# Kernel optimization log

Measured on AMD Instinct MI355X. Metric: run time of the kernel, lower is better.

Reference implementation:

```python
import jax, jax.numpy as jnp
import numpy as np

B, S, D_IN, D_OUT, H = 4, 2048, 1024, 1024, 16
HD = D_OUT // H


def setup_inputs() -> dict:
    key = jax.random.key(0)
    ks = jax.random.split(key, 6)
    s_in = 1.0 / np.sqrt(D_IN)
    s_out = 1.0 / np.sqrt(D_OUT)
    return {
        "x": jax.random.normal(ks[0], (B, S, D_IN), dtype=jnp.float32),
        "Wq": jax.random.uniform(ks[1], (D_IN, D_OUT), jnp.float32, -s_in, s_in),
        "Wk": jax.random.uniform(ks[2], (D_IN, D_OUT), jnp.float32, -s_in, s_in),
        "Wv": jax.random.uniform(ks[3], (D_IN, D_OUT), jnp.float32, -s_in, s_in),
        "Wo": jax.random.uniform(ks[4], (D_OUT, D_OUT), jnp.float32, -s_out, s_out),
        "bo": jax.random.uniform(ks[5], (D_OUT,), jnp.float32, -s_out, s_out),
    }


def reference(x, Wq, Wk, Wv, Wo, bo):
    b, s, _ = x.shape
    # project and split heads: (b, h, s, hd)
    def heads(w):
        return (x @ w).reshape(b, s, H, HD).transpose(0, 2, 1, 3)
    q, k, v = heads(Wq), heads(Wk), heads(Wv)
    scores = jnp.einsum("bhqd,bhkd->bhqk", q, k) / np.sqrt(HD).astype(np.float32)
    causal = jnp.tril(jnp.ones((s, s), dtype=bool))  # True = keep
    scores = jnp.where(causal, scores, -jnp.inf)
    attn = jax.nn.softmax(scores, axis=-1)
    ctx = jnp.einsum("bhqk,bhkd->bhqd", attn, v)
    ctx = ctx.transpose(0, 2, 1, 3).reshape(b, s, D_OUT)
    return ctx @ Wo.T + bo
```

## Files before the change

kernel.cpp:

```cpp
#include <hip/hip_runtime.h>
#include <hip/hip_bf16.h>

#define BB   4
#define SS   2048
#define DIN  1024
#define DOUT 1024
#define NH   16
#define HDIM 64

typedef __hip_bfloat16 bf16;
typedef __attribute__((ext_vector_type(8))) short short8;
typedef __attribute__((ext_vector_type(4))) float floatx4;

#define AS1(p) ((const __attribute__((address_space(1))) void*)(p))
#define AS3(p) ((__attribute__((address_space(3))) void*)(p))

__global__ void cast_f32_bf16_kernel(const float* __restrict__ src, bf16* __restrict__ dst) {
    size_t i = ((size_t)blockIdx.x * 256 + threadIdx.x) * 8;
    float4 a = *(const float4*)(src + i);
    float4 b = *(const float4*)(src + i + 4);
    bf16 o[8] __attribute__((aligned(16)));
    o[0] = __float2bfloat16(a.x); o[1] = __float2bfloat16(a.y);
    o[2] = __float2bfloat16(a.z); o[3] = __float2bfloat16(a.w);
    o[4] = __float2bfloat16(b.x); o[5] = __float2bfloat16(b.y);
    o[6] = __float2bfloat16(b.z); o[7] = __float2bfloat16(b.w);
    *(short8*)(dst + i) = *(short8*)o;
}

__global__ void prep_wqkv_kernel(const float* __restrict__ Wq, const float* __restrict__ Wk,
                                 const float* __restrict__ Wv, bf16* __restrict__ wt) {
    __shared__ float tile[64][65];
    const int kt = blockIdx.x;
    const int nt = blockIdx.y;
    const int k0 = kt * 64, n0 = nt * 64;
    const float* W = (n0 < 1024) ? Wq : (n0 < 2048 ? Wk : Wv);
    const int col0 = n0 & 1023;
    const int tid = threadIdx.x;
    {
        const int kl = tid >> 2, nc = (tid & 3) * 16;
        const float* src = W + (size_t)(k0 + kl) * 1024 + col0 + nc;
        #pragma unroll
        for (int i = 0; i < 16; i += 4) {
            float4 v = *(const float4*)(src + i);
            tile[kl][nc + i + 0] = v.x; tile[kl][nc + i + 1] = v.y;
            tile[kl][nc + i + 2] = v.z; tile[kl][nc + i + 3] = v.w;
        }
    }
    __syncthreads();
    {
        const int nl = tid >> 2, kc = (tid & 3) * 16;
        bf16 o[16] __attribute__((aligned(16)));
        #pragma unroll
        for (int i = 0; i < 16; ++i) o[i] = __float2bfloat16(tile[kc + i][nl]);
        bf16* dst = wt + (size_t)(n0 + nl) * 1024 + k0 + kc;
        *(short8*)dst       = *(short8*)&o[0];
        *(short8*)(dst + 8) = *(short8*)&o[8];
    }
}

template<int EPI>
__global__ __launch_bounds__(256) void gemm_bt_kernel(
    const bf16* __restrict__ A, const bf16* __restrict__ Bt,
    void* __restrict__ C, const float* __restrict__ bias, int K, int ldc) {
    __shared__ __align__(16) bf16 As[128][32];
    __shared__ __align__(16) bf16 Bs[128][32];
    const int tid  = threadIdx.x;
    const int wave = tid >> 6, lane = tid & 63;
    const int lm   = lane & 15, quad = lane >> 4;
    const int wm   = (wave >> 1) * 64, wn = (wave & 1) * 64;
    const size_t rowA0 = (size_t)blockIdx.x * 128;
    const size_t rowB0 = (size_t)blockIdx.y * 128;
    const int srow = wave * 16 + (lane >> 2);
    const int skc  = (lane & 3) * 8;

    floatx4 acc[4][4] = {};

    for (int k0 = 0; k0 < K; k0 += 32) {
        __syncthreads();
        #pragma unroll
        for (int r = 0; r < 2; ++r) {
            const bf16* gA = A  + (rowA0 + r * 64 + srow) * (size_t)K + k0 + skc;
            __builtin_amdgcn_global_load_lds(AS1(gA), AS3(&As[r * 64 + wave * 16][0]), 16, 0, 0);
            const bf16* gB = Bt + (rowB0 + r * 64 + srow) * (size_t)K + k0 + skc;
            __builtin_amdgcn_global_load_lds(AS1(gB), AS3(&Bs[r * 64 + wave * 16][0]), 16, 0, 0);
        }
        __syncthreads();
        short8 a[4], b[4];
        #pragma unroll
        for (int i = 0; i < 4; ++i) a[i] = *(const short8*)&As[wm + i * 16 + lm][quad * 8];
        #pragma unroll
        for (int j = 0; j < 4; ++j) b[j] = *(const short8*)&Bs[wn + j * 16 + lm][quad * 8];
        #pragma unroll
        for (int i = 0; i < 4; ++i)
            #pragma unroll
            for (int j = 0; j < 4; ++j)
                acc[i][j] = __builtin_amdgcn_mfma_f32_16x16x32_bf16(a[i], b[j], acc[i][j], 0, 0, 0);
    }

    #pragma unroll
    for (int i = 0; i < 4; ++i) {
        size_t row = rowA0 + wm + i * 16 + quad * 4;
        #pragma unroll
        for (int j = 0; j < 4; ++j) {
            size_t col = rowB0 + wn + j * 16 + lm;
            float bv = (EPI == 1) ? bias[col] : 0.0f;
            #pragma unroll
            for (int r = 0; r < 4; ++r) {
                if (EPI == 0)
                    ((bf16*)C)[(row + r) * ldc + col] = __float2bfloat16(acc[i][j][r]);
                else
                    ((float*)C)[(row + r) * ldc + col] = acc[i][j][r] + bv;
            }
        }
    }
}

__global__ void transpose_v_kernel(const bf16* __restrict__ qkv, bf16* __restrict__ vt) {
    __shared__ __align__(16) bf16 tile[64][72];
    const int st = blockIdx.x;
    const int bh = blockIdx.y;
    const int b = bh >> 4, h = bh & 15;
    const int s0 = st * 64;
    const int tid = threadIdx.x;
    {
        const int sl = tid >> 2, hc = (tid & 3) * 16;
        const bf16* src = qkv + ((size_t)(b * SS + s0 + sl)) * 3072 + 2048 + h * 64 + hc;
        *(short8*)&tile[sl][hc]     = *(const short8*)src;
        *(short8*)&tile[sl][hc + 8] = *(const short8*)(src + 8);
    }
    __syncthreads();
    {
        const int hl = tid >> 2, sc = (tid & 3) * 16;
        bf16 o[16] __attribute__((aligned(16)));
        #pragma unroll
        for (int i = 0; i < 16; ++i) o[i] = tile[sc + i][hl];
        bf16* dst = vt + ((size_t)(bh * 64 + hl)) * SS + s0 + sc;
        *(short8*)dst       = *(short8*)&o[0];
        *(short8*)(dst + 8) = *(short8*)&o[8];
    }
}

#define PSTR 68
__global__ __launch_bounds__(256, 2) void flash_attn_kernel(
    const bf16* __restrict__ qkv, const bf16* __restrict__ vt, bf16* __restrict__ ctx) {
    __shared__ __align__(16) bf16 Ks[2][64 * 64];
    __shared__ __align__(16) bf16 Vs[2][64 * 64];
    __shared__ __align__(16) bf16 Pl[4][32 * PSTR + 8];
    const int tid  = threadIdx.x;
    const int wave = tid >> 6, lane = tid & 63;
    const int lm   = lane & 15, quad = lane >> 4;

    const int id  = blockIdx.x;
    const int j   = id >> 3;
    const int bh  = (id & 7) * 8 + (j & 7);
    const int p0  = j >> 3;
    const int b = bh >> 4, h = bh & 15;

    const int lane8r = lane >> 3;
    const int schunk = (lane & 7) ^ lane8r;

    const bf16* kg = qkv + (size_t)b * SS * 3072 + 1024 + h * 64 + schunk * 8;
    const bf16* vg = vt + (size_t)(b * NH + h) * 64 * SS + schunk * 8;

    bf16* Pw = &Pl[wave][0];

    #pragma unroll 1
    for (int ph = 0; ph < 2; ++ph) {
        const int p = ph ? (15 - p0) : p0;
        const int qb = p * 128 + wave * 32;
        const int nkt = 2 * p + 2;

        short8 bq[2][2];
        #pragma unroll
        for (int g = 0; g < 2; ++g) {
            const bf16* qp = qkv + ((size_t)(b * SS + qb + g * 16 + lm)) * 3072 + h * 64 + quad * 8;
            bq[g][0] = *(const short8*)qp;
            bq[g][1] = *(const short8*)(qp + 32);
        }

        floatx4 o[2][4] = {};
        float lsum[2] = {0.f, 0.f};

        if (ph) __syncthreads();
        #pragma unroll
        for (int c = 0; c < 2; ++c) {
            const int row = c * 32 + wave * 8 + lane8r;
            __builtin_amdgcn_global_load_lds(AS1(kg + (size_t)row * 3072), AS3(&Ks[0][(c * 256 + wave * 64) * 8]), 16, 0, 0);
            __builtin_amdgcn_global_load_lds(AS1(vg + (size_t)row * SS), AS3(&Vs[0][(c * 256 + wave * 64) * 8]), 16, 0, 0);
        }

        #pragma unroll 1
        for (int kt = 0; kt < nkt; ++kt) {
            const int cur = kt & 1;
            __syncthreads();
            if (kt + 1 < nkt) {
                #pragma unroll
                for (int c = 0; c < 2; ++c) {
                    const int row = c * 32 + wave * 8 + lane8r;
                    __builtin_amdgcn_global_load_lds(AS1(kg + (size_t)((kt + 1) * 64 + row) * 3072),
                                                     AS3(&Ks[cur ^ 1][(c * 256 + wave * 64) * 8]), 16, 0, 0);
                    __builtin_amdgcn_global_load_lds(AS1(vg + (size_t)row * SS + (kt + 1) * 64),
                                                     AS3(&Vs[cur ^ 1][(c * 256 + wave * 64) * 8]), 16, 0, 0);
                }
            }

            const int sw = lm & 7;
            const bf16* Ksb = &Ks[cur][0];
            const bf16* Vsb = &Vs[cur][0];
            short8 ka[4][2], va[4][2];
            #pragma unroll
            for (int nt = 0; nt < 4; ++nt) {
                const int r0 = (nt * 16 + lm) * 64;
                ka[nt][0] = *(const short8*)(Ksb + r0 + ((quad ^ sw) * 8));
                ka[nt][1] = *(const short8*)(Ksb + r0 + (((4 + quad) ^ sw) * 8));
                va[nt][0] = *(const short8*)(Vsb + r0 + ((quad ^ sw) * 8));
                va[nt][1] = *(const short8*)(Vsb + r0 + (((4 + quad) ^ sw) * 8));
            }

            #pragma unroll
            for (int g = 0; g < 2; ++g) {
                floatx4 sc[4];
                #pragma unroll
                for (int nt = 0; nt < 4; ++nt) {
                    floatx4 z = {};
                    z = __builtin_amdgcn_mfma_f32_16x16x32_bf16(ka[nt][0], bq[g][0], z, 0, 0, 0);
                    z = __builtin_amdgcn_mfma_f32_16x16x32_bf16(ka[nt][1], bq[g][1], z, 0, 0, 0);
                    sc[nt] = z;
                }
                if (kt * 64 + 63 > qb + g * 16) {
                    const int qrow = qb + g * 16 + lm;
                    #pragma unroll
                    for (int nt = 0; nt < 4; ++nt)
                        #pragma unroll
                        for (int r = 0; r < 4; ++r)
                            if (kt * 64 + nt * 16 + quad * 4 + r > qrow) sc[nt][r] = -1e30f;
                }
                #pragma unroll
                for (int nt = 0; nt < 4; ++nt) {
                    bf16 pk[4] __attribute__((aligned(8)));
                    #pragma unroll
                    for (int r = 0; r < 4; ++r) {
                        float pv = __builtin_amdgcn_exp2f(sc[nt][r] * 0.18033688f);
                        lsum[g] += pv;
                        pk[r] = __float2bfloat16(pv);
                    }
                    *(uint64_t*)&Pw[(g * 16 + lm) * PSTR + nt * 16 + quad * 4] = *(uint64_t*)pk;
                }
            }
            #pragma unroll
            for (int g = 0; g < 2; ++g) {
                const short8 ap0 = *(const short8*)&Pw[(g * 16 + lm) * PSTR + quad * 8];
                const short8 ap1 = *(const short8*)&Pw[(g * 16 + lm) * PSTR + 32 + quad * 8];
                #pragma unroll
                for (int t = 0; t < 4; ++t) {
                    o[g][t] = __builtin_amdgcn_mfma_f32_16x16x32_bf16(ap0, va[t][0], o[g][t], 0, 0, 0);
                    o[g][t] = __builtin_amdgcn_mfma_f32_16x16x32_bf16(ap1, va[t][1], o[g][t], 0, 0, 0);
                }
            }
        }

        #pragma unroll
        for (int g = 0; g < 2; ++g) {
            float rsum = lsum[g];
            rsum += __shfl_xor(rsum, 16);
            rsum += __shfl_xor(rsum, 32);
            float rl[4];
            #pragma unroll
            for (int r = 0; r < 4; ++r) rl[r] = 1.0f / __shfl(rsum, quad * 4 + r);
            #pragma unroll
            for (int t = 0; t < 4; ++t)
                #pragma unroll
                for (int r = 0; r < 4; ++r) {
                    size_t row = (size_t)b * SS + qb + g * 16 + quad * 4 + r;
                    ctx[row * 1024 + h * 64 + t * 16 + lm] = __float2bfloat16(o[g][t][r] * rl[r]);
                }
        }
    }
}

extern "C" void kernel_launch(void* const* d_in, const int* in_sizes, int n_in,
                              void* d_out, int out_size, void* d_ws, size_t ws_size,
                              hipStream_t stream) {
    const float* x  = (const float*)d_in[0];
    const float* Wq = (const float*)d_in[1];
    const float* Wk = (const float*)d_in[2];
    const float* Wv = (const float*)d_in[3];
    const float* Wo = (const float*)d_in[4];
    const float* bo = (const float*)d_in[5];

    char* ws = (char*)d_ws;
    bf16* xb  = (bf16*)ws;  ws += (size_t)8192 * 1024 * 2;
    bf16* wt  = (bf16*)ws;  ws += (size_t)3072 * 1024 * 2;
    bf16* wob = (bf16*)ws;  ws += (size_t)1024 * 1024 * 2;
    bf16* qkv = (bf16*)ws;  ws += (size_t)8192 * 3072 * 2;
    bf16* vtb = (bf16*)ws;  ws += (size_t)BB * NH * HDIM * SS * 2;
    bf16* ctx = xb;

    cast_f32_bf16_kernel<<<4096, 256, 0, stream>>>(x, xb);
    prep_wqkv_kernel<<<dim3(16, 48), 256, 0, stream>>>(Wq, Wk, Wv, wt);
    cast_f32_bf16_kernel<<<512, 256, 0, stream>>>(Wo, wob);
    gemm_bt_kernel<0><<<dim3(64, 24), 256, 0, stream>>>(xb, wt, (void*)qkv, nullptr, 1024, 3072);
    transpose_v_kernel<<<dim3(32, 64), 256, 0, stream>>>(qkv, vtb);
    flash_attn_kernel<<<512, 256, 0, stream>>>(qkv, vtb, ctx);
    gemm_bt_kernel<1><<<dim3(64, 8), 256, 0, stream>>>(ctx, wob, d_out, bo, 1024, 1024);
}
```

Baseline: 273.1 us.

## Restructure flash attention to two waves with 64 query rows each and skip masked tiles

The attention block shrinks from four waves to two, and each wave now owns 64 query rows (four 16-row groups). This doubles the reuse of the K/V fragments read from LDS per wave. Key tiles past a wave's diagonal are skipped, masking runs only on the diagonal tile, and the P scratch buffer is cut to one 16-row group per wave. The two separate f32-to-bf16 cast launches for x and Wo are also merged into one kernel to save a launch. In exchange, each block has fewer waves to hide latency, registers per wave go up, and the wave that finishes early sits idle at the barriers.

Result: slower. 281.5 us (+3.1%).

```diff
diff --git a/kernel.cpp b/kernel.cpp
--- a/kernel.cpp
+++ b/kernel.cpp
@@ -15,15 +15,20 @@
 #define AS1(p) ((const __attribute__((address_space(1))) void*)(p))
 #define AS3(p) ((__attribute__((address_space(3))) void*)(p))
 
-__global__ void cast_f32_bf16_kernel(const float* __restrict__ src, bf16* __restrict__ dst) {
-    size_t i = ((size_t)blockIdx.x * 256 + threadIdx.x) * 8;
-    float4 a = *(const float4*)(src + i);
-    float4 b = *(const float4*)(src + i + 4);
+__global__ void cast2_kernel(const float* __restrict__ a, bf16* __restrict__ da,
+                             const float* __restrict__ wb, bf16* __restrict__ db, int nba) {
+    const int blk = blockIdx.x;
+    const float* src = (blk < nba) ? a : wb;
+    bf16* dst = (blk < nba) ? da : db;
+    const int rb = (blk < nba) ? blk : blk - nba;
+    size_t i = ((size_t)rb * 256 + threadIdx.x) * 8;
+    float4 x = *(const float4*)(src + i);
+    float4 y = *(const float4*)(src + i + 4);
     bf16 o[8] __attribute__((aligned(16)));
-    o[0] = __float2bfloat16(a.x); o[1] = __float2bfloat16(a.y);
-    o[2] = __float2bfloat16(a.z); o[3] = __float2bfloat16(a.w);
-    o[4] = __float2bfloat16(b.x); o[5] = __float2bfloat16(b.y);
-    o[6] = __float2bfloat16(b.z); o[7] = __float2bfloat16(b.w);
+    o[0] = __float2bfloat16(x.x); o[1] = __float2bfloat16(x.y);
+    o[2] = __float2bfloat16(x.z); o[3] = __float2bfloat16(x.w);
+    o[4] = __float2bfloat16(y.x); o[5] = __float2bfloat16(y.y);
+    o[6] = __float2bfloat16(y.z); o[7] = __float2bfloat16(y.w);
     *(short8*)(dst + i) = *(short8*)o;
 }
 
@@ -141,52 +146,52 @@
 }
 
 #define PSTR 68
-__global__ __launch_bounds__(256, 2) void flash_attn_kernel(
+__global__ __launch_bounds__(128) void flash_attn_kernel(
     const bf16* __restrict__ qkv, const bf16* __restrict__ vt, bf16* __restrict__ ctx) {
     __shared__ __align__(16) bf16 Ks[2][64 * 64];
     __shared__ __align__(16) bf16 Vs[2][64 * 64];
-    __shared__ __align__(16) bf16 Pl[4][32 * PSTR + 8];
+    __shared__ __align__(16) bf16 Pl[2][16 * PSTR + 8];
     const int tid  = threadIdx.x;
     const int wave = tid >> 6, lane = tid & 63;
     const int lm   = lane & 15, quad = lane >> 4;
 
-    const int id  = blockIdx.x;
-    const int j   = id >> 3;
-    const int bh  = (id & 7) * 8 + (j & 7);
-    const int p0  = j >> 3;
+    const int id = blockIdx.x;
+    const int bh = (id & 7) * 8 + ((id >> 3) & 7);
+    const int p0 = id >> 6;
     const int b = bh >> 4, h = bh & 15;
 
     const int lane8r = lane >> 3;
     const int schunk = (lane & 7) ^ lane8r;
+    const int sw = lm & 7;
 
     const bf16* kg = qkv + (size_t)b * SS * 3072 + 1024 + h * 64 + schunk * 8;
     const bf16* vg = vt + (size_t)(b * NH + h) * 64 * SS + schunk * 8;
-
     bf16* Pw = &Pl[wave][0];
 
     #pragma unroll 1
     for (int ph = 0; ph < 2; ++ph) {
-        const int p = ph ? (15 - p0) : p0;
-        const int qb = p * 128 + wave * 32;
-        const int nkt = 2 * p + 2;
-
-        short8 bq[2][2];
-        #pragma unroll
-        for (int g = 0; g < 2; ++g) {
-            const bf16* qp = qkv + ((size_t)(b * SS + qb + g * 16 + lm)) * 3072 + h * 64 + quad * 8;
+        const int p    = ph ? (15 - p0) : p0;
+        const int q0w  = p * 128 + wave * 64;
+        const int diag = q0w >> 6;
+        const int nkt  = 2 * p + 2;
+
+        short8 bq[4][2];
+        #pragma unroll
+        for (int g = 0; g < 4; ++g) {
+            const bf16* qp = qkv + ((size_t)(b * SS + q0w + g * 16 + lm)) * 3072 + h * 64 + quad * 8;
             bq[g][0] = *(const short8*)qp;
             bq[g][1] = *(const short8*)(qp + 32);
         }
 
-        floatx4 o[2][4] = {};
-        float lsum[2] = {0.f, 0.f};
+        floatx4 o[4][4] = {};
+        float lsum[4] = {0.f, 0.f, 0.f, 0.f};
 
         if (ph) __syncthreads();
         #pragma unroll
-        for (int c = 0; c < 2; ++c) {
-            const int row = c * 32 + wave * 8 + lane8r;
-            __builtin_amdgcn_global_load_lds(AS1(kg + (size_t)row * 3072), AS3(&Ks[0][(c * 256 + wave * 64) * 8]), 16, 0, 0);
-            __builtin_amdgcn_global_load_lds(AS1(vg + (size_t)row * SS), AS3(&Vs[0][(c * 256 + wave * 64) * 8]), 16, 0, 0);
+        for (int c = 0; c < 4; ++c) {
+            const int row = c * 16 + wave * 8 + lane8r;
+            __builtin_amdgcn_global_load_lds(AS1(kg + (size_t)row * 3072), AS3(&Ks[0][(c * 16 + wave * 8) * 64]), 16, 0, 0);
+            __builtin_amdgcn_global_load_lds(AS1(vg + (size_t)row * SS),   AS3(&Vs[0][(c * 16 + wave * 8) * 64]), 16, 0, 0);
         }
 
         #pragma unroll 1
@@ -195,16 +200,16 @@
             __syncthreads();
             if (kt + 1 < nkt) {
                 #pragma unroll
-                for (int c = 0; c < 2; ++c) {
-                    const int row = c * 32 + wave * 8 + lane8r;
+                for (int c = 0; c < 4; ++c) {
+                    const int row = c * 16 + wave * 8 + lane8r;
                     __builtin_amdgcn_global_load_lds(AS1(kg + (size_t)((kt + 1) * 64 + row) * 3072),
-                                                     AS3(&Ks[cur ^ 1][(c * 256 + wave * 64) * 8]), 16, 0, 0);
+                                                     AS3(&Ks[cur ^ 1][(c * 16 + wave * 8) * 64]), 16, 0, 0);
                     __builtin_amdgcn_global_load_lds(AS1(vg + (size_t)row * SS + (kt + 1) * 64),
-                                                     AS3(&Vs[cur ^ 1][(c * 256 + wave * 64) * 8]), 16, 0, 0);
+                                                     AS3(&Vs[cur ^ 1][(c * 16 + wave * 8) * 64]), 16, 0, 0);
                 }
             }
-
-            const int sw = lm & 7;
+            if (kt > diag) continue;
+
             const bf16* Ksb = &Ks[cur][0];
             const bf16* Vsb = &Vs[cur][0];
             short8 ka[4][2], va[4][2];
@@ -216,9 +221,10 @@
                 va[nt][0] = *(const short8*)(Vsb + r0 + ((quad ^ sw) * 8));
                 va[nt][1] = *(const short8*)(Vsb + r0 + (((4 + quad) ^ sw) * 8));
             }
-
-            #pragma unroll
-            for (int g = 0; g < 2; ++g) {
+            const bool do_mask = (kt == diag);
+
+            #pragma unroll
+            for (int g = 0; g < 4; ++g) {
                 floatx4 sc[4];
                 #pragma unroll
                 for (int nt = 0; nt < 4; ++nt) {
@@ -227,13 +233,12 @@
                     z = __builtin_amdgcn_mfma_f32_16x16x32_bf16(ka[nt][1], bq[g][1], z, 0, 0, 0);
                     sc[nt] = z;
                 }
-                if (kt * 64 + 63 > qb + g * 16) {
-                    const int qrow = qb + g * 16 + lm;
+                if (do_mask) {
                     #pragma unroll
                     for (int nt = 0; nt < 4; ++nt)
                         #pragma unroll
                         for (int r = 0; r < 4; ++r)
-                            if (kt * 64 + nt * 16 + quad * 4 + r > qrow) sc[nt][r] = -1e30f;
+                            if (nt * 16 + quad * 4 + r > g * 16 + lm) sc[nt][r] = -1e30f;
                 }
                 #pragma unroll
                 for (int nt = 0; nt < 4; ++nt) {
@@ -244,13 +249,10 @@
                         lsum[g] += pv;
                         pk[r] = __float2bfloat16(pv);
                     }
-                    *(uint64_t*)&Pw[(g * 16 + lm) * PSTR + nt * 16 + quad * 4] = *(uint64_t*)pk;
-                }
-            }
-            #pragma unroll
-            for (int g = 0; g < 2; ++g) {
-                const short8 ap0 = *(const short8*)&Pw[(g * 16 + lm) * PSTR + quad * 8];
-                const short8 ap1 = *(const short8*)&Pw[(g * 16 + lm) * PSTR + 32 + quad * 8];
+                    *(uint64_t*)&Pw[lm * PSTR + nt * 16 + quad * 4] = *(uint64_t*)pk;
+                }
+                const short8 ap0 = *(const short8*)&Pw[lm * PSTR + quad * 8];
+                const short8 ap1 = *(const short8*)&Pw[lm * PSTR + 32 + quad * 8];
                 #pragma unroll
                 for (int t = 0; t < 4; ++t) {
                     o[g][t] = __builtin_amdgcn_mfma_f32_16x16x32_bf16(ap0, va[t][0], o[g][t], 0, 0, 0);
@@ -260,7 +262,7 @@
         }
 
         #pragma unroll
-        for (int g = 0; g < 2; ++g) {
+        for (int g = 0; g < 4; ++g) {
             float rsum = lsum[g];
             rsum += __shfl_xor(rsum, 16);
             rsum += __shfl_xor(rsum, 32);
@@ -271,7 +273,7 @@
             for (int t = 0; t < 4; ++t)
                 #pragma unroll
                 for (int r = 0; r < 4; ++r) {
-                    size_t row = (size_t)b * SS + qb + g * 16 + quad * 4 + r;
+                    size_t row = (size_t)b * SS + q0w + g * 16 + quad * 4 + r;
                     ctx[row * 1024 + h * 64 + t * 16 + lm] = __float2bfloat16(o[g][t][r] * rl[r]);
                 }
         }
@@ -296,11 +298,10 @@
     bf16* vtb = (bf16*)ws;  ws += (size_t)BB * NH * HDIM * SS * 2;
     bf16* ctx = xb;
 
-    cast_f32_bf16_kernel<<<4096, 256, 0, stream>>>(x, xb);
+    cast2_kernel<<<4608, 256, 0, stream>>>(x, xb, Wo, wob, 4096);
     prep_wqkv_kernel<<<dim3(16, 48), 256, 0, stream>>>(Wq, Wk, Wv, wt);
-    cast_f32_bf16_kernel<<<512, 256, 0, stream>>>(Wo, wob);
     gemm_bt_kernel<0><<<dim3(64, 24), 256, 0, stream>>>(xb, wt, (void*)qkv, nullptr, 1024, 3072);
     transpose_v_kernel<<<dim3(32, 64), 256, 0, stream>>>(qkv, vtb);
-    flash_attn_kernel<<<512, 256, 0, stream>>>(qkv, vtb, ctx);
+    flash_attn_kernel<<<512, 128, 0, stream>>>(qkv, vtb, ctx);
     gemm_bt_kernel<1><<<dim3(64, 8), 256, 0, stream>>>(ctx, wob, d_out, bo, 1024, 1024);
 }
```
